# Optimization experiments

Hardware: AMD Instinct MI355X
Metric: run time of the kernel (lower is better)

Reference implementation:

```python
import jax, jax.numpy as jnp
import numpy as np
import math

B, L = 4, 2048
D_MODEL, N_HEADS, D_K, D_V, D_FF, FACTOR = 512, 8, 64, 64, 2048, 5


def _layernorm(x, g, b, eps=1e-5):
    m = x.mean(-1, keepdims=True)
    v = jnp.mean((x - m) ** 2, axis=-1, keepdims=True)
    return (x - m) * jax.lax.rsqrt(v + eps) * g + b


def setup_inputs() -> dict:
    key = jax.random.key(0)
    ks = jax.random.split(key, 8)
    w = lambda k, shape: (jax.random.normal(k, shape, jnp.float32) * 0.02)
    sample_k = min(FACTOR * int(math.ceil(math.log(L))), L)  # c*ln(L_K) sampled keys per query
    return {
        "x": jax.random.normal(ks[0], (B, L, D_MODEL), jnp.float32),
        "Wq": w(ks[1], (D_MODEL, N_HEADS * D_K)),
        "Wk": w(ks[2], (D_MODEL, N_HEADS * D_K)),
        "Wv": w(ks[3], (D_MODEL, N_HEADS * D_V)),
        "Wo": w(ks[4], (N_HEADS * D_V, D_MODEL)),
        "ln1_g": jnp.ones((D_MODEL,), jnp.float32),
        "ln1_b": jnp.zeros((D_MODEL,), jnp.float32),
        "conv1_w": w(ks[5], (D_FF, D_MODEL)),
        "conv1_b": jnp.zeros((D_FF,), jnp.float32),
        "conv2_w": w(ks[6], (D_MODEL, D_FF)),
        "conv2_b": jnp.zeros((D_MODEL,), jnp.float32),
        "ln2_g": jnp.ones((D_MODEL,), jnp.float32),
        "ln2_b": jnp.zeros((D_MODEL,), jnp.float32),
        # Informer samples sample_k random keys per query position (constant indices)
        "sample_idx": jax.random.randint(ks[7], (L, sample_k), 0, L),
    }


def reference(x, Wq, Wk, Wv, Wo, ln1_g, ln1_b, conv1_w, conv1_b, conv2_w, conv2_b, ln2_g, ln2_b, sample_idx):
    Bx, Lx, D = x.shape
    H = N_HEADS
    # projections -> [B,H,L,d]
    Q = (x @ Wq).reshape(Bx, Lx, H, D_K).transpose(0, 2, 1, 3)
    K = (x @ Wk).reshape(Bx, Lx, H, D_K).transpose(0, 2, 1, 3)
    V = (x @ Wv).reshape(Bx, Lx, H, D_V).transpose(0, 2, 1, 3)

    u = min(FACTOR * int(math.ceil(math.log(Lx))), Lx)  # top-u active queries
    # sampled QK scores: [B,H,L,sample_k]
    K_samp = K[:, :, sample_idx]                              # [B,H,L,S,dk]
    qk_s = jnp.einsum('bhle,bhlse->bhls', Q, K_samp)
    # sparsity measure M = max - mean (Informer divides sum by L_K)
    M = qk_s.max(-1) - qk_s.sum(-1) / Lx                      # [B,H,L]
    _, top = jax.lax.top_k(M, u)                              # [B,H,u]

    Q_red = jnp.take_along_axis(Q, top[..., None], axis=2)    # [B,H,u,dk]
    scores = jnp.einsum('bhue,bhle->bhul', Q_red, K) / math.sqrt(D_K)
    attn = jax.nn.softmax(scores, axis=-1)                    # [B,H,u,L]

    # initial context = mean of V over keys; update only top-u query rows
    ctx = jnp.broadcast_to(V.mean(axis=2, keepdims=True), V.shape)  # [B,H,L,dv]
    upd = jnp.einsum('bhul,bhld->bhud', attn, V)              # [B,H,u,dv]
    bi = jnp.arange(Bx)[:, None, None]
    hi = jnp.arange(H)[None, :, None]
    ctx = ctx.at[bi, hi, top].set(upd)

    out = ctx.transpose(0, 2, 1, 3).reshape(Bx, Lx, H * D_V) @ Wo
    x1 = _layernorm(x + out, ln1_g, ln1_b)  # residual + norm inside attention sublayer

    # conv1d(k=1) FFN == per-token linear; dropout is identity in eval
    y = jax.nn.gelu(x1 @ conv1_w.T + conv1_b, approximate=False)
    y = y @ conv2_w.T + conv2_b
    return _layernorm(x1 + y, ln2_g, ln2_b)
```

## Files before the change

kernel.cpp:

```cpp
#include <hip/hip_runtime.h>
#include <hip/hip_bf16.h>

#define BB 4
#define LL 2048
#define DD 512
#define HH 8
#define DKK 64
#define FF 2048

typedef __bf16  bf16x8  __attribute__((ext_vector_type(8)));
typedef float   floatx4 __attribute__((ext_vector_type(4)));

__device__ __forceinline__ void async_cp16(const void* g, void* l) {
    __builtin_amdgcn_global_load_lds(
        (const __attribute__((address_space(1))) unsigned int*)g,
        (__attribute__((address_space(3))) unsigned int*)l,
        16, 0, 0);
}

__device__ __forceinline__ float gelu_f(float v) {
    float z  = v * 0.70710678118654752f;
    float az = fabsf(z);
    float t  = __builtin_amdgcn_rcpf(1.0f + 0.3275911f * az);
    float p  = ((((1.061405429f * t - 1.453152027f) * t + 1.421413741f) * t
                 - 0.284496736f) * t + 0.254829592f) * t;
    float e  = __expf(-z * z);
    float er = 1.0f - p * e;
    er = (z < 0.0f) ? -er : er;
    return 0.5f * v * (1.0f + er);
}

__global__ __launch_bounds__(256) void prep_w(
    const float* __restrict__ Wq, const float* __restrict__ Wk,
    const float* __restrict__ Wv, const float* __restrict__ Wo,
    __bf16* __restrict__ wb)
{
    const size_t SZ = (size_t)DD * DD;
    int z = blockIdx.z;
    const float* s = (z == 0) ? Wq : (z == 1) ? Wk : (z == 2) ? Wv : Wo;
    __bf16* hi; __bf16* lo = nullptr;
    if (z == 0)      { hi = wb;          lo = wb + SZ; }
    else if (z == 1) { hi = wb + 2 * SZ; lo = wb + 3 * SZ; }
    else if (z == 2) { hi = wb + 4 * SZ; }
    else             { hi = wb + 5 * SZ; }
    int idx = blockIdx.x * 256 + threadIdx.x;
    int k = idx >> 9, n = idx & 511;
    float v = s[idx];
    __bf16 h = (__bf16)v;
    hi[(size_t)n * DD + k] = h;
    if (lo) lo[(size_t)n * DD + k] = (__bf16)(v - (float)h);
}

__global__ __launch_bounds__(256) void cast_cw(
    const float* __restrict__ c1w, const float* __restrict__ c2w,
    __bf16* __restrict__ d1, __bf16* __restrict__ d2)
{
    const float* s = blockIdx.z ? c2w : c1w;
    __bf16* d = blockIdx.z ? d2 : d1;
    int idx = blockIdx.x * 256 + threadIdx.x;
    d[idx] = (__bf16)s[idx];
}

__global__ __launch_bounds__(256) void split_cast_x(
    const float* __restrict__ x, __bf16* __restrict__ xhi, __bf16* __restrict__ xlo)
{
    int idx = blockIdx.x * 256 + threadIdx.x;
    float v = x[idx];
    __bf16 h = (__bf16)v;
    xhi[idx] = h;
    xlo[idx] = (__bf16)(v - (float)h);
}

template<int ACT, bool BIAS, bool OUT_BF16>
__global__ __launch_bounds__(256) void gemm_mfma(
    const __bf16* __restrict__ A, const __bf16* __restrict__ B,
    const float* __restrict__ bias, void* __restrict__ Cv,
    int M, int N, int K)
{
    __shared__ __bf16 As[3][128 * 32];
    __shared__ __bf16 Bs[3][128 * 32];
    const int tid = threadIdx.x;
    const int wave = tid >> 6, lane = tid & 63;
    const int gx = gridDim.x;
    const int nwg = gx * gridDim.y;
    const int hw = blockIdx.y * gx + blockIdx.x;
    const int virt = ((nwg & 7) == 0) ? ((hw & 7) * (nwg >> 3) + (hw >> 3)) : hw;
    const int m0 = (virt / gx) * 128, n0 = (virt % gx) * 128;
    const int wm = (wave >> 1) * 64, wn = (wave & 1) * 64;
    const int l15 = lane & 15, kq = lane >> 4;

    auto stage = [&](int buf, int k0) {
        #pragma unroll
        for (int p = 0; p < 2; p++) {
            int c = p * 256 + tid;
            int row = c >> 2;
            int col = ((c & 3) ^ ((row >> 1) & 3)) * 8;
            async_cp16(A + (size_t)(m0 + row) * K + k0 + col, &As[buf][c * 8]);
            async_cp16(B + (size_t)(n0 + row) * K + k0 + col, &Bs[buf][c * 8]);
        }
    };

    floatx4 acc[4][4] = {};

    const int nt = K >> 5;
    stage(0, 0);
    stage(1, 32);
    asm volatile("s_waitcnt vmcnt(4)" ::: "memory");
    __builtin_amdgcn_s_barrier();
    int bi = 0;
    for (int t = 0; t < nt; t++) {
        int k2 = (t + 2) << 5;
        if (k2 < K) {
            int b2 = bi + 2; if (b2 >= 3) b2 -= 3;
            stage(b2, k2);
        }
        asm volatile("" ::: "memory");
        bf16x8 af[4], bfr[4];
        #pragma unroll
        for (int i = 0; i < 4; i++) {
            int ra = wm + i * 16 + l15;
            af[i] = *(const bf16x8*)(&As[bi][ra * 32 + ((kq ^ ((ra >> 1) & 3)) << 3)]);
        }
        #pragma unroll
        for (int j = 0; j < 4; j++) {
            int rb = wn + j * 16 + l15;
            bfr[j] = *(const bf16x8*)(&Bs[bi][rb * 32 + ((kq ^ ((rb >> 1) & 3)) << 3)]);
        }
        #pragma unroll
        for (int i = 0; i < 4; i++)
            #pragma unroll
            for (int j = 0; j < 4; j++)
                acc[i][j] = __builtin_amdgcn_mfma_f32_16x16x32_bf16(bfr[j], af[i], acc[i][j], 0, 0, 0);
        asm volatile("" ::: "memory");
        if (t + 2 < nt)      asm volatile("s_waitcnt vmcnt(4)" ::: "memory");
        else if (t + 1 < nt) asm volatile("s_waitcnt vmcnt(0)" ::: "memory");
        if (t + 1 < nt) __builtin_amdgcn_s_barrier();
        if (++bi == 3) bi = 0;
    }
    #pragma unroll
    for (int i = 0; i < 4; i++) {
        int m = m0 + wm + i * 16 + l15;
        #pragma unroll
        for (int j = 0; j < 4; j++) {
            int n = n0 + wn + j * 16 + kq * 4;
            floatx4 v4 = acc[i][j];
            if (BIAS) {
                float4 bv = *(const float4*)&bias[n];
                v4[0] += bv.x; v4[1] += bv.y; v4[2] += bv.z; v4[3] += bv.w;
            }
            if (ACT == 1) {
                v4[0] = gelu_f(v4[0]); v4[1] = gelu_f(v4[1]);
                v4[2] = gelu_f(v4[2]); v4[3] = gelu_f(v4[3]);
            }
            if (OUT_BF16) {
                union { __bf16 b[4]; uint2 u; } pk;
                pk.b[0] = (__bf16)v4[0]; pk.b[1] = (__bf16)v4[1];
                pk.b[2] = (__bf16)v4[2]; pk.b[3] = (__bf16)v4[3];
                *(uint2*)((__bf16*)Cv + (size_t)m * N + n) = pk.u;
            } else {
                *(float4*)((float*)Cv + (size_t)m * N + n) = *(float4*)&v4;
            }
        }
    }
}

__global__ __launch_bounds__(256) void gemm_mfma_split(
    const __bf16* __restrict__ Ah, const __bf16* __restrict__ Al,
    const __bf16* __restrict__ Bh, const __bf16* __restrict__ Bl,
    float* __restrict__ C, int M, int N, int K)
{
    __shared__ __bf16 Ahs[3][128 * 32];
    __shared__ __bf16 Als[3][128 * 32];
    __shared__ __bf16 Bhs[3][128 * 32];
    __shared__ __bf16 Bls[3][128 * 32];
    const int tid = threadIdx.x;
    const int wave = tid >> 6, lane = tid & 63;
    const int gx = gridDim.x;
    const int nwg = gx * gridDim.y;
    const int hw = blockIdx.y * gx + blockIdx.x;
    const int virt = ((nwg & 7) == 0) ? ((hw & 7) * (nwg >> 3) + (hw >> 3)) : hw;
    const int m0 = (virt / gx) * 128, n0 = (virt % gx) * 128;
    const int wm = (wave >> 1) * 64, wn = (wave & 1) * 64;
    const int l15 = lane & 15, kq = lane >> 4;

    auto stage = [&](int buf, int k0) {
        #pragma unroll
        for (int p = 0; p < 2; p++) {
            int c = p * 256 + tid;
            int row = c >> 2;
            int col = ((c & 3) ^ ((row >> 1) & 3)) * 8;
            size_t goA = (size_t)(m0 + row) * K + k0 + col;
            size_t goB = (size_t)(n0 + row) * K + k0 + col;
            async_cp16(Ah + goA, &Ahs[buf][c * 8]);
            async_cp16(Al + goA, &Als[buf][c * 8]);
            async_cp16(Bh + goB, &Bhs[buf][c * 8]);
            async_cp16(Bl + goB, &Bls[buf][c * 8]);
        }
    };

    floatx4 acc[4][4] = {};

    const int nt = K >> 5;
    stage(0, 0);
    stage(1, 32);
    asm volatile("s_waitcnt vmcnt(8)" ::: "memory");
    __builtin_amdgcn_s_barrier();
    int bi = 0;
    for (int t = 0; t < nt; t++) {
        int k2 = (t + 2) << 5;
        if (k2 < K) {
            int b2 = bi + 2; if (b2 >= 3) b2 -= 3;
            stage(b2, k2);
        }
        asm volatile("" ::: "memory");
        bf16x8 ah[4], al[4], bh[4], bl[4];
        #pragma unroll
        for (int i = 0; i < 4; i++) {
            int ra = wm + i * 16 + l15;
            int off = ra * 32 + ((kq ^ ((ra >> 1) & 3)) << 3);
            ah[i] = *(const bf16x8*)(&Ahs[bi][off]);
            al[i] = *(const bf16x8*)(&Als[bi][off]);
        }
        #pragma unroll
        for (int j = 0; j < 4; j++) {
            int rb = wn + j * 16 + l15;
            int off = rb * 32 + ((kq ^ ((rb >> 1) & 3)) << 3);
            bh[j] = *(const bf16x8*)(&Bhs[bi][off]);
            bl[j] = *(const bf16x8*)(&Bls[bi][off]);
        }
        #pragma unroll
        for (int i = 0; i < 4; i++)
            #pragma unroll
            for (int j = 0; j < 4; j++) {
                acc[i][j] = __builtin_amdgcn_mfma_f32_16x16x32_bf16(bh[j], ah[i], acc[i][j], 0, 0, 0);
                acc[i][j] = __builtin_amdgcn_mfma_f32_16x16x32_bf16(bl[j], ah[i], acc[i][j], 0, 0, 0);
                acc[i][j] = __builtin_amdgcn_mfma_f32_16x16x32_bf16(bh[j], al[i], acc[i][j], 0, 0, 0);
            }
        asm volatile("" ::: "memory");
        if (t + 2 < nt)      asm volatile("s_waitcnt vmcnt(8)" ::: "memory");
        else if (t + 1 < nt) asm volatile("s_waitcnt vmcnt(0)" ::: "memory");
        if (t + 1 < nt) __builtin_amdgcn_s_barrier();
        if (++bi == 3) bi = 0;
    }
    #pragma unroll
    for (int i = 0; i < 4; i++) {
        int m = m0 + wm + i * 16 + l15;
        #pragma unroll
        for (int j = 0; j < 4; j++) {
            int n = n0 + wn + j * 16 + kq * 4;
            *(float4*)(C + (size_t)m * N + n) = *(float4*)&acc[i][j];
        }
    }
}

__device__ __forceinline__ float dpp_sum16(float p) {
    int t;
    t = __builtin_amdgcn_update_dpp(0, __float_as_int(p), 0xB1,  0xF, 0xF, true);
    p += __int_as_float(t);
    t = __builtin_amdgcn_update_dpp(0, __float_as_int(p), 0x4E,  0xF, 0xF, true);
    p += __int_as_float(t);
    t = __builtin_amdgcn_update_dpp(0, __float_as_int(p), 0x141, 0xF, 0xF, true);
    p += __int_as_float(t);
    t = __builtin_amdgcn_update_dpp(0, __float_as_int(p), 0x140, 0xF, 0xF, true);
    p += __int_as_float(t);
    return p;
}

__global__ __launch_bounds__(256) void calc_m(
    const float* __restrict__ Q, const float* __restrict__ Kb,
    const int* __restrict__ sidx, float* __restrict__ Mo, int U)
{
    __shared__ int   js[64];
    __shared__ float red_mx[2][HH];
    __shared__ float red_sm[2][HH];
    int i = blockIdx.x;
    int b = i & 3, l = i >> 2;
    int tid = threadIdx.x;
    if (tid < U) js[tid] = sidx[l * U + tid];
    int e    = (tid & 127) * 4;
    int slot = tid >> 7;
    const float* qr = Q + ((size_t)(b * LL + l) * DD);
    float4 q = *(const float4*)(qr + e);
    const float* kbase = Kb + ((size_t)b * LL) * DD + e;
    __syncthreads();
    float mx = -1e30f, sm = 0.f;
    for (int s = slot; s < U; s += 2) {
        int j = js[s];
        float4 kv = *(const float4*)(kbase + (size_t)j * DD);
        float p = q.x * kv.x + q.y * kv.y + q.z * kv.z + q.w * kv.w;
        p = dpp_sum16(p);
        mx = fmaxf(mx, p);
        sm += p;
    }
    if ((tid & 15) == 0) {
        int head = (tid >> 4) & 7;
        red_mx[slot][head] = mx;
        red_sm[slot][head] = sm;
    }
    __syncthreads();
    if (tid < HH) {
        float m2 = fmaxf(red_mx[0][tid], red_mx[1][tid]);
        float s2 = red_sm[0][tid] + red_sm[1][tid];
        Mo[((size_t)(b * HH + tid)) * LL + l] = m2 - s2 * (1.0f / (float)LL);
    }
}

__global__ __launch_bounds__(256) void topk_k(
    const float* __restrict__ Mo, int* __restrict__ top, int U)
{
    __shared__ unsigned int hist[256];
    __shared__ unsigned int wsum[4];
    __shared__ unsigned int bc[2];
    __shared__ int ties[LL];
    __shared__ int cnt2[2];
    int bh = blockIdx.x, tid = threadIdx.x;
    int lane = tid & 63, w = tid >> 6;

    unsigned int my[8];
    #pragma unroll
    for (int i = 0; i < 8; i++) {
        unsigned int u = __float_as_uint(Mo[(size_t)bh * LL + tid + i * 256]);
        my[i] = u ^ ((u >> 31) ? 0xFFFFFFFFu : 0x80000000u);
    }

    unsigned int prefix = 0, pmask = 0;
    unsigned int need = (unsigned int)U;
    unsigned int above = 0;

    for (int pass = 0; pass < 4; pass++) {
        int shift = 24 - pass * 8;
        hist[tid] = 0;
        __syncthreads();
        #pragma unroll
        for (int i = 0; i < 8; i++) {
            unsigned int u = my[i];
            if ((u & pmask) == prefix)
                atomicAdd(&hist[(u >> shift) & 255u], 1u);
        }
        __syncthreads();
        unsigned int h = hist[tid];
        #pragma unroll
        for (int off = 1; off < 64; off <<= 1) {
            unsigned int o = __shfl_down(h, off);
            if (lane + off < 64) h += o;
        }
        if (lane == 0) wsum[w] = h;
        __syncthreads();
        unsigned int tail = 0;
        #pragma unroll
        for (int w2 = 1; w2 < 4; w2++) if (w2 > w) tail += wsum[w2];
        h += tail;
        hist[tid] = h;
        __syncthreads();
        unsigned int St = h;
        unsigned int St1 = (tid < 255) ? hist[tid + 1] : 0u;
        if (St >= need && St1 < need) { bc[0] = (unsigned int)tid; bc[1] = St1; }
        __syncthreads();
        unsigned int dig = bc[0], abv = bc[1];
        above += abv;
        need -= abv;
        prefix |= dig << shift;
        pmask |= 0xFFu << shift;
        __syncthreads();
    }

    if (tid == 0) { cnt2[0] = 0; cnt2[1] = 0; }
    __syncthreads();
    #pragma unroll
    for (int i = 0; i < 8; i++) {
        unsigned int u = my[i];
        int idx = tid + i * 256;
        if (u > prefix) {
            int pos = atomicAdd(&cnt2[0], 1);
            top[bh * U + pos] = idx;
        } else if (u == prefix) {
            int pos = atomicAdd(&cnt2[1], 1);
            ties[pos] = idx;
        }
    }
    __syncthreads();
    int tcnt = cnt2[1];
    #pragma unroll
    for (int i = 0; i < 8; i++) {
        unsigned int u = my[i];
        if (u == prefix) {
            int idx = tid + i * 256;
            int rank = 0;
            for (int j = 0; j < tcnt; j++) rank += (ties[j] < idx) ? 1 : 0;
            if (rank < (int)need) top[bh * U + (int)above + rank] = idx;
        }
    }
}

__global__ __launch_bounds__(256) void vmean_k(
    const __bf16* __restrict__ V, float* __restrict__ Vm)
{
    __shared__ float osum[4][DKK];
    int bh = blockIdx.x;
    int b = bh >> 3, h = bh & 7;
    int tid = threadIdx.x, d = tid & 63, part = tid >> 6;
    const __bf16* vp = V + ((size_t)(b * LL + part * 512) * DD + h * DKK + d);
    float s = 0.f;
    for (int i = 0; i < 512; i++) s += (float)vp[(size_t)i * DD];
    osum[part][d] = s;
    __syncthreads();
    if (tid < DKK)
        Vm[bh * DKK + tid] = (osum[0][tid] + osum[1][tid] + osum[2][tid] + osum[3][tid]) * (1.0f / (float)LL);
}

__global__ __launch_bounds__(256) void gather_qred(
    const float* __restrict__ Q, const int* __restrict__ top,
    __bf16* __restrict__ qred, int U)
{
    int bh = blockIdx.y;
    int b = bh >> 3, h = bh & 7;
    int e = blockIdx.x * 256 + threadIdx.x;
    int u = e >> 6, d = e & 63;
    float v = 0.f;
    if (u < U) {
        int l = top[bh * U + u];
        v = Q[((size_t)(b * LL + l) * DD + h * DKK) + d] * 0.125f;
    }
    qred[(size_t)bh * 48 * DKK + e] = (__bf16)v;
}

__global__ __launch_bounds__(256) void gemm_s(
    const __bf16* __restrict__ qred, const float* __restrict__ Kb,
    float* __restrict__ S)
{
    __shared__ __bf16 Qs[2 * 48 * 32];
    __shared__ __bf16 Ks[2 * 128 * 32];
    int bh = blockIdx.y, nc = blockIdx.x;
    int b = bh >> 3, h = bh & 7, l0 = nc * 128;
    int tid = threadIdx.x;
    const unsigned int* qsrc = (const unsigned int*)(qred + (size_t)bh * 48 * DKK);
    unsigned int* qdst = (unsigned int*)Qs;
    #pragma unroll
    for (int t = 0; t < 6; t++) {
        int ui = tid + t * 256;
        int u = ui >> 5, kp = ui & 31;
        int p = kp >> 4, kl2 = kp & 15;
        qdst[p * 768 + u * 16 + kl2] = qsrc[ui];
    }
    #pragma unroll
    for (int t = 0; t < 8; t++) {
        int fi = tid + t * 256;
        int row = fi >> 4, k4 = fi & 15;
        int p = k4 >> 3, kl = (k4 & 7) * 4;
        float4 kv = *(const float4*)(Kb + ((size_t)(b * LL + l0 + row) * DD + h * DKK + k4 * 4));
        __bf16* dst = Ks + p * 128 * 32 + row * 32 + kl;
        dst[0] = (__bf16)kv.x; dst[1] = (__bf16)kv.y;
        dst[2] = (__bf16)kv.z; dst[3] = (__bf16)kv.w;
    }
    __syncthreads();
    int wave = tid >> 6, lane = tid & 63, l15 = lane & 15, kq = lane >> 4;
    floatx4 acc[3][2] = {};
    #pragma unroll
    for (int p = 0; p < 2; p++) {
        bf16x8 bq[2];
        #pragma unroll
        for (int j = 0; j < 2; j++)
            bq[j] = *(const bf16x8*)(Ks + p * 4096 + (wave * 32 + j * 16 + l15) * 32 + kq * 8);
        #pragma unroll
        for (int i = 0; i < 3; i++) {
            bf16x8 aq = *(const bf16x8*)(Qs + p * 1536 + (i * 16 + l15) * 32 + kq * 8);
            #pragma unroll
            for (int j = 0; j < 2; j++)
                acc[i][j] = __builtin_amdgcn_mfma_f32_16x16x32_bf16(bq[j], aq, acc[i][j], 0, 0, 0);
        }
    }
    #pragma unroll
    for (int i = 0; i < 3; i++) {
        int row = i * 16 + l15;
        #pragma unroll
        for (int j = 0; j < 2; j++) {
            int col = l0 + wave * 32 + j * 16 + kq * 4;
            *(float4*)&S[((size_t)bh * 48 + row) * LL + col] = *(float4*)&acc[i][j];
        }
    }
}

__global__ __launch_bounds__(256) void softmax_p(float* __restrict__ S, int U)
{
    __shared__ float red[256];
    int row = blockIdx.x;
    int bh = row / U, u = row % U;
    float* sr = S + ((size_t)bh * 48 + u) * LL;
    int tid = threadIdx.x;
    float sc[8]; float mx = -1e30f;
    #pragma unroll
    for (int i = 0; i < 8; i++) { sc[i] = sr[tid + i * 256]; mx = fmaxf(mx, sc[i]); }
    red[tid] = mx; __syncthreads();
    for (int s = 128; s > 0; s >>= 1) { if (tid < s) red[tid] = fmaxf(red[tid], red[tid + s]); __syncthreads(); }
    mx = red[0]; __syncthreads();
    float se = 0.f;
    #pragma unroll
    for (int i = 0; i < 8; i++) { sc[i] = __expf(sc[i] - mx); se += sc[i]; }
    red[tid] = se; __syncthreads();
    for (int s = 128; s > 0; s >>= 1) { if (tid < s) red[tid] += red[tid + s]; __syncthreads(); }
    float inv = 1.0f / red[0];
    __bf16* pr = (__bf16*)sr;
    #pragma unroll
    for (int i = 0; i < 8; i++) pr[tid + i * 256] = (__bf16)(sc[i] * inv);
}

__global__ __launch_bounds__(256) void pv_k(
    const float* __restrict__ S, const __bf16* __restrict__ V,
    float* __restrict__ upd, int U)
{
    __shared__ __bf16 pls[4 * LL];
    __shared__ float osum[4][4][DKK];
    int bh = blockIdx.y, uc = blockIdx.x;
    int b = bh >> 3, h = bh & 7, tid = threadIdx.x;
    #pragma unroll
    for (int t = 0; t < 16; t++) {
        int ui = tid + t * 256;
        int up = ui >> 10, lw = ui & 1023;
        const unsigned int* src = (const unsigned int*)(S + ((size_t)bh * 48 + uc * 4 + up) * LL);
        ((unsigned int*)pls)[up * 1024 + lw] = src[lw];
    }
    __syncthreads();
    int d = tid & 63, part = tid >> 6;
    float a0 = 0.f, a1 = 0.f, a2 = 0.f, a3 = 0.f;
    const __bf16* vp = V + ((size_t)(b * LL + part * 512) * DD + h * DKK + d);
    int lbase = part * 512;
    for (int i = 0; i < 512; i++) {
        float v = (float)vp[(size_t)i * DD];
        int l = lbase + i;
        a0 += (float)pls[l] * v;
        a1 += (float)pls[LL + l] * v;
        a2 += (float)pls[2 * LL + l] * v;
        a3 += (float)pls[3 * LL + l] * v;
    }
    osum[part][0][d] = a0; osum[part][1][d] = a1;
    osum[part][2][d] = a2; osum[part][3][d] = a3;
    __syncthreads();
    int u2 = tid >> 6;
    float s = osum[0][u2][d] + osum[1][u2][d] + osum[2][u2][d] + osum[3][u2][d];
    upd[((size_t)bh * U + uc * 4 + u2) * DKK + d] = s;
}

__global__ __launch_bounds__(256) void base_k(
    const float* __restrict__ Vm, const float* __restrict__ Wo,
    float* __restrict__ base)
{
    __shared__ float cm[DD];
    __shared__ float part[8][32];
    int b = blockIdx.y, n0 = blockIdx.x * 32, tid = threadIdx.x;
    cm[tid] = Vm[b * DD + tid];
    cm[tid + 256] = Vm[b * DD + 256 + tid];
    __syncthreads();
    int n = n0 + (tid & 31), kg = tid >> 5;
    float s = 0.f;
    for (int k = kg * 64; k < kg * 64 + 64; k++) s += cm[k] * Wo[(size_t)k * DD + n];
    part[kg][tid & 31] = s;
    __syncthreads();
    if (tid < 32) {
        float t = 0.f;
        #pragma unroll
        for (int g = 0; g < 8; g++) t += part[g][tid];
        base[b * DD + n0 + tid] = t;
    }
}

__global__ __launch_bounds__(256) void aout_init(
    const float* __restrict__ base, float* __restrict__ aout)
{
    int idx = blockIdx.x * 256 + threadIdx.x;
    aout[idx] = base[((idx >> 20) << 9) + (idx & 511)];
}

__global__ __launch_bounds__(256) void aw_prep(
    const float* __restrict__ upd, const float* __restrict__ Vm,
    __bf16* __restrict__ aw, int U)
{
    int bh = blockIdx.x, tid = threadIdx.x;
    #pragma unroll
    for (int t = 0; t < 12; t++) {
        int e = tid + t * 256;
        int u = e >> 6, d = e & 63;
        float v = (u < U) ? upd[((size_t)bh * U + u) * DKK + d] - Vm[bh * DKK + d] : 0.f;
        aw[(size_t)bh * 48 * DKK + e] = (__bf16)v;
    }
}

__global__ __launch_bounds__(256) void corr_gemm(
    const __bf16* __restrict__ aw, const __bf16* __restrict__ WoT,
    const int* __restrict__ top, float* __restrict__ aout, int U)
{
    __shared__ __bf16 Qs[2 * 48 * 32];
    __shared__ __bf16 Ks[2 * 128 * 32];
    int bh = blockIdx.y, nc = blockIdx.x;
    int b = bh >> 3, h = bh & 7, n0 = nc * 128;
    int tid = threadIdx.x;
    const unsigned int* qsrc = (const unsigned int*)(aw + (size_t)bh * 48 * DKK);
    unsigned int* qdst = (unsigned int*)Qs;
    #pragma unroll
    for (int t = 0; t < 6; t++) {
        int ui = tid + t * 256;
        int u = ui >> 5, kp = ui & 31;
        int p = kp >> 4, kl2 = kp & 15;
        qdst[p * 768 + u * 16 + kl2] = qsrc[ui];
    }
    const unsigned int* wsrc = (const unsigned int*)WoT;
    unsigned int* kdst = (unsigned int*)Ks;
    #pragma unroll
    for (int t = 0; t < 16; t++) {
        int ui = tid + t * 256;
        int row = ui >> 5, c2 = ui & 31;
        int p = c2 >> 4, col2 = c2 & 15;
        kdst[p * 2048 + row * 16 + col2] = wsrc[(size_t)(n0 + row) * (DD / 2) + h * 32 + c2];
    }
    __syncthreads();
    int wave = tid >> 6, lane = tid & 63, l15 = lane & 15, kq = lane >> 4;
    floatx4 acc[3][2] = {};
    #pragma unroll
    for (int p = 0; p < 2; p++) {
        bf16x8 bq[2];
        #pragma unroll
        for (int j = 0; j < 2; j++)
            bq[j] = *(const bf16x8*)(Ks + p * 4096 + (wave * 32 + j * 16 + l15) * 32 + kq * 8);
        #pragma unroll
        for (int i = 0; i < 3; i++) {
            bf16x8 aq = *(const bf16x8*)(Qs + p * 1536 + (i * 16 + l15) * 32 + kq * 8);
            #pragma unroll
            for (int j = 0; j < 2; j++)
                acc[i][j] = __builtin_amdgcn_mfma_f32_16x16x32_bf16(bq[j], aq, acc[i][j], 0, 0, 0);
        }
    }
    #pragma unroll
    for (int i = 0; i < 3; i++) {
        int u = i * 16 + l15;
        if (u < U) {
            int l = top[bh * U + u];
            float* dst = aout + ((size_t)(b * LL + l)) * DD;
            #pragma unroll
            for (int j = 0; j < 2; j++) {
                int n = n0 + wave * 32 + j * 16 + kq * 4;
                atomicAdd(dst + n,     acc[i][j][0]);
                atomicAdd(dst + n + 1, acc[i][j][1]);
                atomicAdd(dst + n + 2, acc[i][j][2]);
                atomicAdd(dst + n + 3, acc[i][j][3]);
            }
        }
    }
}

__global__ __launch_bounds__(256) void ln1_k(
    const float* __restrict__ x, const float* __restrict__ aout,
    const float* __restrict__ g, const float* __restrict__ bb,
    __bf16* __restrict__ x1h)
{
    __shared__ float red[256];
    int row = blockIdx.x, tid = threadIdx.x;
    size_t base = (size_t)row * DD;
    float h0 = x[base + tid] + aout[base + tid];
    float h1 = x[base + 256 + tid] + aout[base + 256 + tid];
    red[tid] = h0 + h1; __syncthreads();
    for (int s = 128; s > 0; s >>= 1) { if (tid < s) red[tid] += red[tid + s]; __syncthreads(); }
    float mean = red[0] * (1.0f / DD); __syncthreads();
    float d0 = h0 - mean, d1 = h1 - mean;
    red[tid] = d0 * d0 + d1 * d1; __syncthreads();
    for (int s = 128; s > 0; s >>= 1) { if (tid < s) red[tid] += red[tid + s]; __syncthreads(); }
    float rstd = rsqrtf(red[0] * (1.0f / DD) + 1e-5f);
    x1h[base + tid]       = (__bf16)(d0 * rstd * g[tid] + bb[tid]);
    x1h[base + 256 + tid] = (__bf16)(d1 * rstd * g[256 + tid] + bb[256 + tid]);
}

__global__ __launch_bounds__(256) void ln2_k(
    const __bf16* __restrict__ x1h, const float* __restrict__ f2o,
    const float* __restrict__ c2b,
    const float* __restrict__ g, const float* __restrict__ bb,
    float* __restrict__ out)
{
    __shared__ float red[256];
    int row = blockIdx.x, tid = threadIdx.x;
    size_t base = (size_t)row * DD;
    float h0 = (float)x1h[base + tid] + f2o[base + tid] + c2b[tid];
    float h1 = (float)x1h[base + 256 + tid] + f2o[base + 256 + tid] + c2b[256 + tid];
    red[tid] = h0 + h1; __syncthreads();
    for (int s = 128; s > 0; s >>= 1) { if (tid < s) red[tid] += red[tid + s]; __syncthreads(); }
    float mean = red[0] * (1.0f / DD); __syncthreads();
    float d0 = h0 - mean, d1 = h1 - mean;
    red[tid] = d0 * d0 + d1 * d1; __syncthreads();
    for (int s = 128; s > 0; s >>= 1) { if (tid < s) red[tid] += red[tid + s]; __syncthreads(); }
    float rstd = rsqrtf(red[0] * (1.0f / DD) + 1e-5f);
    out[base + tid]       = d0 * rstd * g[tid] + bb[tid];
    out[base + 256 + tid] = d1 * rstd * g[256 + tid] + bb[256 + tid];
}

extern "C" void kernel_launch(void* const* d_in, const int* in_sizes, int n_in,
                              void* d_out, int out_size, void* d_ws, size_t ws_size,
                              hipStream_t stream)
{
    const float* x   = (const float*)d_in[0];
    const float* Wq  = (const float*)d_in[1];
    const float* Wk  = (const float*)d_in[2];
    const float* Wv  = (const float*)d_in[3];
    const float* Wo  = (const float*)d_in[4];
    const float* g1  = (const float*)d_in[5];
    const float* b1  = (const float*)d_in[6];
    const float* c1w = (const float*)d_in[7];
    const float* c1b = (const float*)d_in[8];
    const float* c2w = (const float*)d_in[9];
    const float* c2b = (const float*)d_in[10];
    const float* g2  = (const float*)d_in[11];
    const float* b2  = (const float*)d_in[12];
    const int* sidx  = (const int*)d_in[13];
    float* out       = (float*)d_out;

    const int U = in_sizes[13] / LL;
    const int M = BB * LL;

    char* ws = (char*)d_ws;
    const size_t MB = (size_t)1 << 20;
    float*  Q    = (float*)(ws + 0);
    float*  Kb   = (float*)(ws + 16 * MB);
    __bf16* V    = (__bf16*)(ws + 32 * MB);
    __bf16* xhi  = (__bf16*)(ws + 40 * MB);
    __bf16* xlo  = (__bf16*)(ws + 48 * MB);
    float*  S    = (float*)(ws + 40 * MB);
    __bf16* wb   = (__bf16*)(ws + 56 * MB);
    __bf16* c1wb = (__bf16*)(ws + 59 * MB);
    __bf16* c2wb = (__bf16*)(ws + 61 * MB);
    float*  Mo   = (float*)(ws + 63 * MB);
    float*  upd  = (float*)(ws + 63 * MB + 256 * 1024);
    float*  Vm   = (float*)(ws + 63 * MB + 576 * 1024);
    int*    top  = (int*)  (ws + 63 * MB + 584 * 1024);
    __bf16* qred = (__bf16*)(ws + 63 * MB + 592 * 1024);
    __bf16* aw   = (__bf16*)(ws + 63 * MB + 784 * 1024);
    float*  basep= (float*)(ws + 63 * MB + 976 * 1024);
    float*  aout = Q;
    float*  f2o  = Q;
    __bf16* ych  = (__bf16*)(ws + 16 * MB);
    __bf16* x1h  = xlo;
    (void)ws_size; (void)n_in; (void)out_size;

    const size_t SZ = (size_t)DD * DD;
    __bf16* WqThi = wb;          __bf16* WqTlo = wb + SZ;
    __bf16* WkThi = wb + 2 * SZ; __bf16* WkTlo = wb + 3 * SZ;
    __bf16* WvT   = wb + 4 * SZ; __bf16* WoT   = wb + 5 * SZ;

    prep_w<<<dim3(DD * DD / 256, 1, 4), 256, 0, stream>>>(Wq, Wk, Wv, Wo, wb);
    cast_cw<<<dim3(FF * DD / 256, 1, 2), 256, 0, stream>>>(c1w, c2w, c1wb, c2wb);
    split_cast_x<<<BB * LL * DD / 256, 256, 0, stream>>>(x, xhi, xlo);

    dim3 gproj(DD / 128, M / 128);
    gemm_mfma_split<<<gproj, 256, 0, stream>>>(xhi, xlo, WqThi, WqTlo, Q,  M, DD, DD);
    gemm_mfma_split<<<gproj, 256, 0, stream>>>(xhi, xlo, WkThi, WkTlo, Kb, M, DD, DD);
    gemm_mfma<0, false, true ><<<gproj, 256, 0, stream>>>(xhi, WvT, nullptr, V, M, DD, DD);

    calc_m<<<BB * LL, 256, 0, stream>>>(Q, Kb, sidx, Mo, U);
    topk_k<<<BB * HH, 256, 0, stream>>>(Mo, top, U);
    vmean_k<<<BB * HH, 256, 0, stream>>>(V, Vm);

    gather_qred<<<dim3(48 * DKK / 256, BB * HH), 256, 0, stream>>>(Q, top, qred, U);
    gemm_s<<<dim3(LL / 128, BB * HH), 256, 0, stream>>>(qred, Kb, S);
    softmax_p<<<BB * HH * U, 256, 0, stream>>>(S, U);
    pv_k<<<dim3(U / 4, BB * HH), 256, 0, stream>>>(S, V, upd, U);

    base_k<<<dim3(16, BB), 256, 0, stream>>>(Vm, Wo, basep);
    aw_prep<<<BB * HH, 256, 0, stream>>>(upd, Vm, aw, U);
    aout_init<<<M * DD / 256, 256, 0, stream>>>(basep, aout);
    corr_gemm<<<dim3(DD / 128, BB * HH), 256, 0, stream>>>(aw, WoT, top, aout, U);

    ln1_k<<<M, 256, 0, stream>>>(x, aout, g1, b1, x1h);

    gemm_mfma<1, true,  true ><<<dim3(FF / 128, M / 128), 256, 0, stream>>>(x1h, c1wb, c1b, ych, M, FF, DD);
    gemm_mfma<0, false, false><<<dim3(DD / 128, M / 128), 256, 0, stream>>>(ych, c2wb, nullptr, f2o, M, DD, FF);

    ln2_k<<<M, 256, 0, stream>>>(x1h, f2o, c2b, g2, b2, out);
}
```

Before: 429.6 us.

## Deepen GEMM prefetch pipelines and split PV over key chunks with atomics

The bf16 GEMM kernel is templated on its LDS buffer depth. It uses 6 stages for the V projection and the FF2 GEMM, keeps 3 for FF1, and the split-precision GEMM moves to 4 stages, with wait counts adjusted to match. The intent is to keep more global loads in flight and hide memory latency on the GEMMs with few workgroups. The PV kernel is also split across 4 key chunks, using vectorized V loads and atomicAdd into a zeroed output, to get more parallelism. The cost is more LDS per block, which may lower occupancy, an extra zeroing launch, and atomic contention.

Result: faster. 399.7 us (-7.0%).

```diff
diff --git a/kernel.cpp b/kernel.cpp
--- a/kernel.cpp
+++ b/kernel.cpp
@@ -71,14 +71,14 @@
     xlo[idx] = (__bf16)(v - (float)h);
 }
 
-template<int ACT, bool BIAS, bool OUT_BF16>
+template<int NB, int ACT, bool BIAS, bool OUT_BF16>
 __global__ __launch_bounds__(256) void gemm_mfma(
     const __bf16* __restrict__ A, const __bf16* __restrict__ B,
     const float* __restrict__ bias, void* __restrict__ Cv,
     int M, int N, int K)
 {
-    __shared__ __bf16 As[3][128 * 32];
-    __shared__ __bf16 Bs[3][128 * 32];
+    __shared__ __bf16 As[NB][128 * 32];
+    __shared__ __bf16 Bs[NB][128 * 32];
     const int tid = threadIdx.x;
     const int wave = tid >> 6, lane = tid & 63;
     const int gx = gridDim.x;
@@ -103,16 +103,16 @@
     floatx4 acc[4][4] = {};
 
     const int nt = K >> 5;
-    stage(0, 0);
-    stage(1, 32);
-    asm volatile("s_waitcnt vmcnt(4)" ::: "memory");
+    #pragma unroll
+    for (int pt = 0; pt < NB - 1; pt++) stage(pt, pt << 5);
+    if constexpr (NB == 6) asm volatile("s_waitcnt vmcnt(16)" ::: "memory");
+    else                   asm volatile("s_waitcnt vmcnt(4)"  ::: "memory");
     __builtin_amdgcn_s_barrier();
     int bi = 0;
     for (int t = 0; t < nt; t++) {
-        int k2 = (t + 2) << 5;
-        if (k2 < K) {
-            int b2 = bi + 2; if (b2 >= 3) b2 -= 3;
-            stage(b2, k2);
+        if (t + NB - 1 < nt) {
+            int b2 = bi + NB - 1; if (b2 >= NB) b2 -= NB;
+            stage(b2, (t + NB - 1) << 5);
         }
         asm volatile("" ::: "memory");
         bf16x8 af[4], bfr[4];
@@ -132,10 +132,16 @@
             for (int j = 0; j < 4; j++)
                 acc[i][j] = __builtin_amdgcn_mfma_f32_16x16x32_bf16(bfr[j], af[i], acc[i][j], 0, 0, 0);
         asm volatile("" ::: "memory");
-        if (t + 2 < nt)      asm volatile("s_waitcnt vmcnt(4)" ::: "memory");
-        else if (t + 1 < nt) asm volatile("s_waitcnt vmcnt(0)" ::: "memory");
-        if (t + 1 < nt) __builtin_amdgcn_s_barrier();
-        if (++bi == 3) bi = 0;
+        if (t + 1 < nt) {
+            int c = nt - 2 - t; if (c > NB - 2) c = NB - 2;
+            if (c >= 4)      asm volatile("s_waitcnt vmcnt(16)" ::: "memory");
+            else if (c == 3) asm volatile("s_waitcnt vmcnt(12)" ::: "memory");
+            else if (c == 2) asm volatile("s_waitcnt vmcnt(8)"  ::: "memory");
+            else if (c == 1) asm volatile("s_waitcnt vmcnt(4)"  ::: "memory");
+            else             asm volatile("s_waitcnt vmcnt(0)"  ::: "memory");
+            __builtin_amdgcn_s_barrier();
+        }
+        if (++bi == NB) bi = 0;
     }
     #pragma unroll
     for (int i = 0; i < 4; i++) {
@@ -169,10 +175,10 @@
     const __bf16* __restrict__ Bh, const __bf16* __restrict__ Bl,
     float* __restrict__ C, int M, int N, int K)
 {
-    __shared__ __bf16 Ahs[3][128 * 32];
-    __shared__ __bf16 Als[3][128 * 32];
-    __shared__ __bf16 Bhs[3][128 * 32];
-    __shared__ __bf16 Bls[3][128 * 32];
+    __shared__ __bf16 Ahs[4][128 * 32];
+    __shared__ __bf16 Als[4][128 * 32];
+    __shared__ __bf16 Bhs[4][128 * 32];
+    __shared__ __bf16 Bls[4][128 * 32];
     const int tid = threadIdx.x;
     const int wave = tid >> 6, lane = tid & 63;
     const int gx = gridDim.x;
@@ -201,16 +207,14 @@
     floatx4 acc[4][4] = {};
 
     const int nt = K >> 5;
-    stage(0, 0);
-    stage(1, 32);
-    asm volatile("s_waitcnt vmcnt(8)" ::: "memory");
+    stage(0, 0); stage(1, 32); stage(2, 64);
+    asm volatile("s_waitcnt vmcnt(16)" ::: "memory");
     __builtin_amdgcn_s_barrier();
     int bi = 0;
     for (int t = 0; t < nt; t++) {
-        int k2 = (t + 2) << 5;
-        if (k2 < K) {
-            int b2 = bi + 2; if (b2 >= 3) b2 -= 3;
-            stage(b2, k2);
+        if (t + 3 < nt) {
+            int b2 = bi + 3; if (b2 >= 4) b2 -= 4;
+            stage(b2, (t + 3) << 5);
         }
         asm volatile("" ::: "memory");
         bf16x8 ah[4], al[4], bh[4], bl[4];
@@ -237,10 +241,14 @@
                 acc[i][j] = __builtin_amdgcn_mfma_f32_16x16x32_bf16(bh[j], al[i], acc[i][j], 0, 0, 0);
             }
         asm volatile("" ::: "memory");
-        if (t + 2 < nt)      asm volatile("s_waitcnt vmcnt(8)" ::: "memory");
-        else if (t + 1 < nt) asm volatile("s_waitcnt vmcnt(0)" ::: "memory");
-        if (t + 1 < nt) __builtin_amdgcn_s_barrier();
-        if (++bi == 3) bi = 0;
+        if (t + 1 < nt) {
+            int c = nt - 2 - t; if (c > 2) c = 2;
+            if (c == 2)      asm volatile("s_waitcnt vmcnt(16)" ::: "memory");
+            else if (c == 1) asm volatile("s_waitcnt vmcnt(8)"  ::: "memory");
+            else             asm volatile("s_waitcnt vmcnt(0)"  ::: "memory");
+            __builtin_amdgcn_s_barrier();
+        }
+        if (++bi == 4) bi = 0;
     }
     #pragma unroll
     for (int i = 0; i < 4; i++) {
@@ -504,40 +512,55 @@
     for (int i = 0; i < 8; i++) pr[tid + i * 256] = (__bf16)(sc[i] * inv);
 }
 
+__global__ __launch_bounds__(256) void zero_upd(float* __restrict__ upd, int n)
+{
+    int i = blockIdx.x * 256 + threadIdx.x;
+    if (i < n) upd[i] = 0.f;
+}
+
 __global__ __launch_bounds__(256) void pv_k(
     const float* __restrict__ S, const __bf16* __restrict__ V,
     float* __restrict__ upd, int U)
 {
-    __shared__ __bf16 pls[4 * LL];
-    __shared__ float osum[4][4][DKK];
-    int bh = blockIdx.y, uc = blockIdx.x;
+    __shared__ __bf16 pls[4][512];
+    __shared__ float osum[16][4][DKK];
+    int uc = blockIdx.x, lc = blockIdx.y, bh = blockIdx.z;
     int b = bh >> 3, h = bh & 7, tid = threadIdx.x;
     #pragma unroll
-    for (int t = 0; t < 16; t++) {
+    for (int t = 0; t < 4; t++) {
         int ui = tid + t * 256;
-        int up = ui >> 10, lw = ui & 1023;
-        const unsigned int* src = (const unsigned int*)(S + ((size_t)bh * 48 + uc * 4 + up) * LL);
-        ((unsigned int*)pls)[up * 1024 + lw] = src[lw];
-    }
-    __syncthreads();
-    int d = tid & 63, part = tid >> 6;
-    float a0 = 0.f, a1 = 0.f, a2 = 0.f, a3 = 0.f;
-    const __bf16* vp = V + ((size_t)(b * LL + part * 512) * DD + h * DKK + d);
-    int lbase = part * 512;
-    for (int i = 0; i < 512; i++) {
-        float v = (float)vp[(size_t)i * DD];
-        int l = lbase + i;
-        a0 += (float)pls[l] * v;
-        a1 += (float)pls[LL + l] * v;
-        a2 += (float)pls[2 * LL + l] * v;
-        a3 += (float)pls[3 * LL + l] * v;
-    }
-    osum[part][0][d] = a0; osum[part][1][d] = a1;
-    osum[part][2][d] = a2; osum[part][3][d] = a3;
-    __syncthreads();
-    int u2 = tid >> 6;
-    float s = osum[0][u2][d] + osum[1][u2][d] + osum[2][u2][d] + osum[3][u2][d];
-    upd[((size_t)bh * U + uc * 4 + u2) * DKK + d] = s;
+        int up = ui >> 8, lw = ui & 255;
+        ((unsigned int*)pls)[up * 256 + lw] =
+            ((const unsigned int*)(S + ((size_t)bh * 48 + uc * 4 + up) * LL))[lc * 256 + lw];
+    }
+    __syncthreads();
+    int d4 = tid & 15, part = tid >> 4;
+    const __bf16* vp = V + ((size_t)(b * LL + lc * 512 + part * 32)) * DD + h * DKK + d4 * 4;
+    float a[4][4] = {};
+    for (int i = 0; i < 32; i++) {
+        union { uint2 u; __bf16 bb[4]; } cv;
+        cv.u = *(const uint2*)(vp + (size_t)i * DD);
+        float v0 = (float)cv.bb[0], v1 = (float)cv.bb[1];
+        float v2 = (float)cv.bb[2], v3 = (float)cv.bb[3];
+        int l = part * 32 + i;
+        #pragma unroll
+        for (int u2 = 0; u2 < 4; u2++) {
+            float p = (float)pls[u2][l];
+            a[u2][0] += p * v0; a[u2][1] += p * v1;
+            a[u2][2] += p * v2; a[u2][3] += p * v3;
+        }
+    }
+    #pragma unroll
+    for (int u2 = 0; u2 < 4; u2++)
+        #pragma unroll
+        for (int j = 0; j < 4; j++)
+            osum[part][u2][d4 * 4 + j] = a[u2][j];
+    __syncthreads();
+    int d = tid & 63, u2 = tid >> 6;
+    float s = 0.f;
+    #pragma unroll
+    for (int p = 0; p < 16; p++) s += osum[p][u2][d];
+    atomicAdd(&upd[((size_t)bh * U + uc * 4 + u2) * DKK + d], s);
 }
 
 __global__ __launch_bounds__(256) void base_k(
@@ -748,16 +771,17 @@
     dim3 gproj(DD / 128, M / 128);
     gemm_mfma_split<<<gproj, 256, 0, stream>>>(xhi, xlo, WqThi, WqTlo, Q,  M, DD, DD);
     gemm_mfma_split<<<gproj, 256, 0, stream>>>(xhi, xlo, WkThi, WkTlo, Kb, M, DD, DD);
-    gemm_mfma<0, false, true ><<<gproj, 256, 0, stream>>>(xhi, WvT, nullptr, V, M, DD, DD);
+    gemm_mfma<6, 0, false, true ><<<gproj, 256, 0, stream>>>(xhi, WvT, nullptr, V, M, DD, DD);
 
     calc_m<<<BB * LL, 256, 0, stream>>>(Q, Kb, sidx, Mo, U);
+    zero_upd<<<(BB * HH * U * DKK + 255) / 256, 256, 0, stream>>>(upd, BB * HH * U * DKK);
     topk_k<<<BB * HH, 256, 0, stream>>>(Mo, top, U);
     vmean_k<<<BB * HH, 256, 0, stream>>>(V, Vm);
 
     gather_qred<<<dim3(48 * DKK / 256, BB * HH), 256, 0, stream>>>(Q, top, qred, U);
     gemm_s<<<dim3(LL / 128, BB * HH), 256, 0, stream>>>(qred, Kb, S);
     softmax_p<<<BB * HH * U, 256, 0, stream>>>(S, U);
-    pv_k<<<dim3(U / 4, BB * HH), 256, 0, stream>>>(S, V, upd, U);
+    pv_k<<<dim3(U / 4, 4, BB * HH), 256, 0, stream>>>(S, V, upd, U);
 
     base_k<<<dim3(16, BB), 256, 0, stream>>>(Vm, Wo, basep);
     aw_prep<<<BB * HH, 256, 0, stream>>>(upd, Vm, aw, U);
@@ -766,8 +790,8 @@
 
     ln1_k<<<M, 256, 0, stream>>>(x, aout, g1, b1, x1h);
 
-    gemm_mfma<1, true,  true ><<<dim3(FF / 128, M / 128), 256, 0, stream>>>(x1h, c1wb, c1b, ych, M, FF, DD);
-    gemm_mfma<0, false, false><<<dim3(DD / 128, M / 128), 256, 0, stream>>>(ych, c2wb, nullptr, f2o, M, DD, FF);
+    gemm_mfma<3, 1, true,  true ><<<dim3(FF / 128, M / 128), 256, 0, stream>>>(x1h, c1wb, c1b, ych, M, FF, DD);
+    gemm_mfma<6, 0, false, false><<<dim3(DD / 128, M / 128), 256, 0, stream>>>(ych, c2wb, nullptr, f2o, M, DD, FF);
 
     ln2_k<<<M, 256, 0, stream>>>(x1h, f2o, c2b, g2, b2, out);
 }
```
